# Kernel tuning notes

Hardware: AMD Instinct MI355X
Metric: run time of the kernel (lower is better)

Reference implementation:

```python
import jax, jax.numpy as jnp
import numpy as np

NUM_GRAPHS = 128
NODES_PER_GRAPH = 512
NUM_NODES = NUM_GRAPHS * NODES_PER_GRAPH
NUM_EDGES = NUM_NODES * 16
IN_DIM = 64
HID = 128
NUM_HEADS = 4
BN_EPS = 1e-5


def setup_inputs() -> dict:
    key = jax.random.key(0)
    ks = jax.random.split(key, 12)
    x = jax.random.normal(ks[0], (NUM_NODES, IN_DIM), dtype=jnp.float32)
    edge_index = jax.random.randint(ks[1], (2, NUM_EDGES), 0, NUM_NODES, dtype=jnp.int32)
    batch = jnp.repeat(jnp.arange(NUM_GRAPHS, dtype=jnp.int32), NODES_PER_GRAPH)
    s = 0.05
    W0 = jax.random.normal(ks[2], (IN_DIM, HID), dtype=jnp.float32) * s
    b0 = jnp.zeros((HID,), jnp.float32)
    Wh = jax.random.normal(ks[3], (3, HID, HID), dtype=jnp.float32) * s  # convs 1..3
    bh = jnp.zeros((3, HID), jnp.float32)
    bn_gamma = jnp.ones((4, HID), jnp.float32)
    bn_beta = jnp.zeros((4, HID), jnp.float32)
    bn_mean = jnp.zeros((4, HID), jnp.float32)
    bn_var = jnp.ones((4, HID), jnp.float32)
    attn_in_w = jax.random.normal(ks[4], (3 * HID, HID), dtype=jnp.float32) * s
    attn_in_b = jnp.zeros((3 * HID,), jnp.float32)
    attn_out_w = jax.random.normal(ks[5], (HID, HID), dtype=jnp.float32) * s
    attn_out_b = jnp.zeros((HID,), jnp.float32)
    return dict(x=x, W0=W0, b0=b0, Wh=Wh, bh=bh, bn_gamma=bn_gamma, bn_beta=bn_beta,
                bn_mean=bn_mean, bn_var=bn_var, attn_in_w=attn_in_w, attn_in_b=attn_in_b,
                attn_out_w=attn_out_w, attn_out_b=attn_out_b, edge_index=edge_index, batch=batch)


def _forward(x, W0, b0, Wh, bh, bn_gamma, bn_beta, bn_mean, bn_var,
             attn_in_w, attn_in_b, attn_out_w, attn_out_b, edge_index, batch):
    N = x.shape[0]
    src, dst = edge_index[0], edge_index[1]
    # GCN symmetric normalization with self-loops (PyG GCNConv)
    deg = jax.ops.segment_sum(jnp.ones_like(src, jnp.float32), dst, num_segments=N) + 1.0
    dis = jax.lax.rsqrt(deg)                      # deg^{-1/2}
    enorm = (dis[src] * dis[dst])[:, None]        # per-edge norm
    self_norm = (dis * dis)[:, None]              # self-loop norm

    def gcn(h, W, b):
        h = h @ W
        agg = jax.ops.segment_sum(h[src] * enorm, dst, num_segments=N)
        return agg + h * self_norm + b

    def bn(h, i):
        scale = bn_gamma[i] * jax.lax.rsqrt(bn_var[i] + BN_EPS)
        return (h - bn_mean[i]) * scale + bn_beta[i]  # eval-mode BN

    # dropout is identity in eval mode
    h = jax.nn.relu(bn(gcn(x, W0, b0), 0))
    h = jax.nn.relu(bn(gcn(h, Wh[0], bh[0]), 1))
    h = jax.nn.relu(bn(gcn(h, Wh[1], bh[1]), 2))
    f = jax.nn.relu(bn(gcn(h, Wh[2], bh[2]), 3))   # [N, HID]

    # per-graph self-attention (equal-size contiguous graphs -> batched MHA)
    dh = HID // NUM_HEADS
    xg = f.reshape(NUM_GRAPHS, NODES_PER_GRAPH, HID)
    qkv = xg @ attn_in_w.T + attn_in_b            # [G, n, 3H]
    q, k, v = jnp.split(qkv, 3, axis=-1)

    def heads(t):
        return t.reshape(NUM_GRAPHS, NODES_PER_GRAPH, NUM_HEADS, dh).transpose(0, 2, 1, 3)
    q, k, v = heads(q), heads(k), heads(v)
    scores = jnp.einsum('ghnd,ghmd->ghnm', q, k) / np.sqrt(dh).astype(np.float32)
    attn = jax.nn.softmax(scores, axis=-1)
    o = jnp.einsum('ghnm,ghmd->ghnd', attn, v).transpose(0, 2, 1, 3).reshape(NUM_GRAPHS, NODES_PER_GRAPH, HID)
    o = o @ attn_out_w.T + attn_out_b
    final = o.reshape(N, HID)

    # global mean pool over batch indices
    cnt = jax.ops.segment_sum(jnp.ones((N,), jnp.float32), batch, num_segments=NUM_GRAPHS)
    graph_emb = jax.ops.segment_sum(final, batch, num_segments=NUM_GRAPHS) / cnt[:, None]
    return final, graph_emb


def reference(x, W0, b0, Wh, bh, bn_gamma, bn_beta, bn_mean, bn_var,
              attn_in_w, attn_in_b, attn_out_w, attn_out_b, edge_index, batch):
    return _forward(x, W0, b0, Wh, bh, bn_gamma, bn_beta, bn_mean, bn_var,
                    attn_in_w, attn_in_b, attn_out_w, attn_out_b, edge_index, batch)
```

## Files before the change

kernel.cpp:

```cpp
#include <hip/hip_runtime.h>
#include <hip/hip_bf16.h>
#include <cstdint>
#include <cstddef>

#define N_NODES 65536
#define N_EDGES 1048576
#define N_GRAPHS 128
#define NPG 512
#define IN_DIM 64
#define HID 128
#define BN_EPS 1e-5f

typedef __attribute__((ext_vector_type(8))) short bf16x8;
typedef __attribute__((ext_vector_type(4))) float f32x4;
typedef __attribute__((ext_vector_type(8))) unsigned short u16x8;

__device__ inline unsigned short f2bf(float f) {
  unsigned u = __builtin_bit_cast(unsigned, f);
  u = u + 0x7fffu + ((u >> 16) & 1u);
  return (unsigned short)(u >> 16);
}
__device__ inline float bf2f(unsigned short h) {
  unsigned u = ((unsigned)h) << 16;
  return __builtin_bit_cast(float, u);
}
__device__ inline void split_bf(float v, unsigned short& hi, unsigned short& lo) {
  hi = f2bf(v);
  lo = f2bf(v - bf2f(hi));
}
__device__ inline void split_bf_fast(float v, unsigned short& hi, unsigned short& lo) {
  unsigned u = __builtin_bit_cast(unsigned, v);
  hi = (unsigned short)(u >> 16);
  float r = v - __builtin_bit_cast(float, u & 0xffff0000u);
  lo = f2bf(r);
}

__global__ __launch_bounds__(256) void hist_kernel(const int* __restrict__ dst,
                                                   int* __restrict__ deg) {
  int e = blockIdx.x * 256 + threadIdx.x;
  if (e < N_EDGES) atomicAdd(&deg[dst[e]], 1);
}

__global__ __launch_bounds__(256) void dis_kernel(const int* __restrict__ deg,
                                                  float* __restrict__ dis) {
  int n = blockIdx.x * 256 + threadIdx.x;
  if (n < N_NODES) dis[n] = 1.0f / sqrtf((float)deg[n] + 1.0f);
}

__global__ __launch_bounds__(1024) void scan_kernel(const int* __restrict__ deg,
                                                    int* __restrict__ offsets,
                                                    int* __restrict__ cursor) {
  __shared__ int sums[1024];
  int t = threadIdx.x;
  int base = t * 64;
  const int4* dp = (const int4*)(deg + base);
  int s = 0;
#pragma unroll
  for (int i = 0; i < 16; i++) {
    int4 v = dp[i];
    s += v.x + v.y + v.z + v.w;
  }
  sums[t] = s;
  __syncthreads();
  for (int off = 1; off < 1024; off <<= 1) {
    int v = (t >= off) ? sums[t - off] : 0;
    __syncthreads();
    sums[t] += v;
    __syncthreads();
  }
  int run = (t == 0) ? 0 : sums[t - 1];
#pragma unroll
  for (int i = 0; i < 16; i++) {
    int4 v = dp[i];
    int idx = base + i * 4;
    offsets[idx] = run; cursor[idx] = run; run += v.x;
    offsets[idx + 1] = run; cursor[idx + 1] = run; run += v.y;
    offsets[idx + 2] = run; cursor[idx + 2] = run; run += v.z;
    offsets[idx + 3] = run; cursor[idx + 3] = run; run += v.w;
  }
  if (t == 1023) offsets[N_NODES] = run;
}

__global__ __launch_bounds__(256) void fill_kernel(const int* __restrict__ src,
                                                   const int* __restrict__ dst,
                                                   int* __restrict__ cursor,
                                                   int* __restrict__ csr) {
  int e = blockIdx.x * 256 + threadIdx.x;
  if (e < N_EDGES) {
    int d = dst[e];
    int slot = atomicAdd(&cursor[d], 1);
    csr[slot] = src[e];
  }
}

__global__ __launch_bounds__(256) void agg64_kernel(const float* __restrict__ x,
                                                    const float* __restrict__ dis,
                                                    const int* __restrict__ offsets,
                                                    const int* __restrict__ csr,
                                                    unsigned short* __restrict__ zhi,
                                                    unsigned short* __restrict__ zlo) {
  int node = blockIdx.x * 4 + (threadIdx.x >> 6);
  int lane = threadIdx.x & 63;
  float dn = dis[node];
  float acc = x[(size_t)node * 64 + lane] * dn * dn;
  int beg = offsets[node], end = offsets[node + 1];
  int k = beg;
  for (; k + 4 <= end; k += 4) {
    int s0 = csr[k], s1 = csr[k + 1], s2 = csr[k + 2], s3 = csr[k + 3];
    float w0 = dn * dis[s0], w1 = dn * dis[s1], w2 = dn * dis[s2], w3 = dn * dis[s3];
    float v0 = x[(size_t)s0 * 64 + lane];
    float v1 = x[(size_t)s1 * 64 + lane];
    float v2 = x[(size_t)s2 * 64 + lane];
    float v3 = x[(size_t)s3 * 64 + lane];
    acc = fmaf(w0, v0, acc);
    acc = fmaf(w1, v1, acc);
    acc = fmaf(w2, v2, acc);
    acc = fmaf(w3, v3, acc);
  }
  for (; k < end; k++) {
    int s = csr[k];
    acc = fmaf(dn * dis[s], x[(size_t)s * 64 + lane], acc);
  }
  unsigned short h_, l_;
  split_bf(acc, h_, l_);
  zhi[(size_t)node * 64 + lane] = h_;
  zlo[(size_t)node * 64 + lane] = l_;
}

__global__ __launch_bounds__(256) void agg128_kernel(const float* __restrict__ h,
                                                     const float* __restrict__ dis,
                                                     const int* __restrict__ offsets,
                                                     const int* __restrict__ csr,
                                                     unsigned short* __restrict__ zhi,
                                                     unsigned short* __restrict__ zlo) {
  int node = blockIdx.x * 4 + (threadIdx.x >> 6);
  int lane = threadIdx.x & 63;
  float dn = dis[node];
  float sn = dn * dn;
  const float* hr = h + (size_t)node * 128;
  float a0 = hr[lane] * sn;
  float a1 = hr[lane + 64] * sn;
  int beg = offsets[node], end = offsets[node + 1];
  int k = beg;
  for (; k + 4 <= end; k += 4) {
    int s0 = csr[k], s1 = csr[k + 1], s2 = csr[k + 2], s3 = csr[k + 3];
    float w0 = dn * dis[s0], w1 = dn * dis[s1], w2 = dn * dis[s2], w3 = dn * dis[s3];
    const float* p0 = h + (size_t)s0 * 128;
    const float* p1 = h + (size_t)s1 * 128;
    const float* p2 = h + (size_t)s2 * 128;
    const float* p3 = h + (size_t)s3 * 128;
    float u0 = p0[lane], d0 = p0[lane + 64];
    float u1 = p1[lane], d1 = p1[lane + 64];
    float u2 = p2[lane], d2 = p2[lane + 64];
    float u3 = p3[lane], d3 = p3[lane + 64];
    a0 = fmaf(w0, u0, a0); a1 = fmaf(w0, d0, a1);
    a0 = fmaf(w1, u1, a0); a1 = fmaf(w1, d1, a1);
    a0 = fmaf(w2, u2, a0); a1 = fmaf(w2, d2, a1);
    a0 = fmaf(w3, u3, a0); a1 = fmaf(w3, d3, a1);
  }
  for (; k < end; k++) {
    int s = csr[k];
    float w = dn * dis[s];
    const float* hs = h + (size_t)s * 128;
    a0 = fmaf(w, hs[lane], a0);
    a1 = fmaf(w, hs[lane + 64], a1);
  }
  unsigned short h0, l0, h1, l1;
  split_bf(a0, h0, l0);
  split_bf(a1, h1, l1);
  zhi[(size_t)node * 128 + lane] = h0;
  zlo[(size_t)node * 128 + lane] = l0;
  zhi[(size_t)node * 128 + lane + 64] = h1;
  zlo[(size_t)node * 128 + lane + 64] = l1;
}

template <bool TRANS>
__global__ __launch_bounds__(256) void wprep_kernel(const float* __restrict__ W, int K, int O,
                                                    unsigned short* __restrict__ hi,
                                                    unsigned short* __restrict__ lo) {
  int idx = blockIdx.x * 256 + threadIdx.x;
  int KC = K / 32;
  int total = (O / 16) * KC * 64;
  if (idx >= total) return;
  int lane = idx & 63;
  int rest = idx >> 6;
  int kc = rest % KC;
  int nt = rest / KC;
  int n = nt * 16 + (lane & 15);
  int kb = kc * 32 + (lane >> 4) * 8;
  unsigned short* hp = hi + (size_t)idx * 8;
  unsigned short* lp = lo + (size_t)idx * 8;
#pragma unroll
  for (int j = 0; j < 8; j++) {
    int k = kb + j;
    float v = TRANS ? W[(size_t)n * K + k] : W[(size_t)k * O + n];
    unsigned short h_, l_;
    split_bf(v, h_, l_);
    hp[j] = h_;
    lp[j] = l_;
  }
}

template <int K, int O, bool DOBN, bool DORELU, bool SPLIT_OUT, bool GROUPED>
__global__ __launch_bounds__(256) void gemm_mfma(
    const unsigned short* __restrict__ Ahi, const unsigned short* __restrict__ Alo,
    const unsigned short* __restrict__ Whi, const unsigned short* __restrict__ Wlo,
    const float* __restrict__ bias,
    const float* __restrict__ gamma, const float* __restrict__ beta,
    const float* __restrict__ mean, const float* __restrict__ var,
    float* __restrict__ Cf, unsigned short* __restrict__ Chi,
    unsigned short* __restrict__ Clo) {
  constexpr int KC = K / 32;
  int wave = threadIdx.x >> 6;
  int lane = threadIdx.x & 63;
  int m0 = blockIdx.x * 128 + wave * 32;
  int o0 = blockIdx.y * 128;
  int mrow = lane & 15;
  int kseg = (lane >> 4) * 8;

  f32x4 acc[2][8];
#pragma unroll
  for (int mt = 0; mt < 2; mt++)
#pragma unroll
    for (int nt = 0; nt < 8; nt++) acc[mt][nt] = (f32x4)0.0f;

#pragma unroll
  for (int kc = 0; kc < KC; kc++) {
    bf16x8 ah[2], al[2];
#pragma unroll
    for (int mt = 0; mt < 2; mt++) {
      size_t aoff = (size_t)(m0 + mt * 16 + mrow) * K + kc * 32 + kseg;
      ah[mt] = *(const bf16x8*)(Ahi + aoff);
      al[mt] = *(const bf16x8*)(Alo + aoff);
    }
#pragma unroll
    for (int nt = 0; nt < 8; nt++) {
      size_t foff = (((size_t)(blockIdx.y * 8 + nt) * KC + kc) * 64 + lane) * 8;
      bf16x8 bh = *(const bf16x8*)(Whi + foff);
      bf16x8 bl = *(const bf16x8*)(Wlo + foff);
#pragma unroll
      for (int mt = 0; mt < 2; mt++) {
        acc[mt][nt] = __builtin_amdgcn_mfma_f32_16x16x32_bf16(ah[mt], bh, acc[mt][nt], 0, 0, 0);
        acc[mt][nt] = __builtin_amdgcn_mfma_f32_16x16x32_bf16(ah[mt], bl, acc[mt][nt], 0, 0, 0);
        acc[mt][nt] = __builtin_amdgcn_mfma_f32_16x16x32_bf16(al[mt], bh, acc[mt][nt], 0, 0, 0);
        acc[mt][nt] = __builtin_amdgcn_mfma_f32_16x16x32_bf16(al[mt], bl, acc[mt][nt], 0, 0, 0);
      }
    }
  }

  int ccol = lane & 15;
  int crow0 = (lane >> 4) * 4;
#pragma unroll
  for (int nt = 0; nt < 8; nt++) {
    int c = o0 + nt * 16 + ccol;
    float sc, cb;
    float b = bias[c];
    if (DOBN) {
      sc = gamma[c] * rsqrtf(var[c] + BN_EPS);
      cb = (b - mean[c]) * sc + beta[c];
    } else {
      sc = 1.0f;
      cb = b;
    }
#pragma unroll
    for (int mt = 0; mt < 2; mt++) {
#pragma unroll
      for (int r = 0; r < 4; r++) {
        float v = fmaf(acc[mt][nt][r], sc, cb);
        if (DORELU) v = fmaxf(v, 0.0f);
        size_t row = (size_t)(m0 + mt * 16 + crow0 + r);
        if (SPLIT_OUT) {
          unsigned short h_, l_;
          split_bf(v, h_, l_);
          if (GROUPED) {
            size_t base = row * (size_t)(2 * O) + (size_t)(((c >> 5) << 6) + (c & 31));
            Chi[base] = h_;
            Chi[base + 32] = l_;
          } else {
            Chi[row * O + c] = h_;
            Clo[row * O + c] = l_;
          }
        } else {
          Cf[row * O + c] = v;
        }
      }
    }
  }
}

__global__ __launch_bounds__(256) void knorm_kernel(const unsigned short* __restrict__ qvs,
                                                    float* __restrict__ kmax2) {
  int g = blockIdx.x >> 2;
  int h = blockIdx.x & 3;
  size_t gbase = (size_t)g * NPG;
  float best = 0.0f;
#pragma unroll
  for (int r = 0; r < 2; r++) {
    int j = r * 256 + threadIdx.x;
    size_t base = (gbase + j) * 768 + (size_t)(4 + h) * 64;
    float s = 0.0f;
#pragma unroll
    for (int i = 0; i < 4; i++) {
      u16x8 hh = *(const u16x8*)(qvs + base + i * 8);
      u16x8 ll = *(const u16x8*)(qvs + base + 32 + i * 8);
#pragma unroll
      for (int jj = 0; jj < 8; jj++) {
        float v = bf2f(hh[jj]) + bf2f(ll[jj]);
        s = fmaf(v, v, s);
      }
    }
    best = fmaxf(best, s);
  }
#pragma unroll
  for (int off = 32; off >= 1; off >>= 1)
    best = fmaxf(best, __shfl_xor(best, off, 64));
  __shared__ float red[4];
  int wave = threadIdx.x >> 6;
  if ((threadIdx.x & 63) == 0) red[wave] = best;
  __syncthreads();
  if (threadIdx.x == 0) {
    float m = fmaxf(fmaxf(red[0], red[1]), fmaxf(red[2], red[3]));
    kmax2[blockIdx.x] = m;
  }
}

__global__ __launch_bounds__(256, 2) void attn_mfma_kernel(
    const unsigned short* __restrict__ qvs, const float* __restrict__ kmax2,
    unsigned short* __restrict__ ohi, unsigned short* __restrict__ olo) {
  int wb = ((blockIdx.x & 7) << 7) | (blockIdx.x >> 3);
  int g = wb >> 3;
  int h = (wb >> 1) & 3;
  int half = wb & 1;
  int t = threadIdx.x;
  int wave = t >> 6;
  int lane = t & 63;
  int quad = lane >> 4;
  int l15 = lane & 15;
  size_t gbase = (size_t)g * NPG;
  int qb = half * 256 + wave * 64;

  const float cf = 0.17677669529663687f * 1.4426950408889634f;

  __shared__ unsigned short Kh[2][32][40] __attribute__((aligned(16)));
  __shared__ unsigned short Kl[2][32][40] __attribute__((aligned(16)));
  __shared__ unsigned short Vh[2][33][40] __attribute__((aligned(16)));
  __shared__ unsigned short Vl[2][33][40] __attribute__((aligned(16)));
  __shared__ char wbuf[4][10240] __attribute__((aligned(16)));

  unsigned short* Ph = (unsigned short*)wbuf[wave];
  unsigned short* Pl = Ph + 64 * 40;
  float* Ot = (float*)wbuf[wave];

  bf16x8 qh[4], ql[4];
  float qn2p[4];
#pragma unroll
  for (int mt = 0; mt < 4; mt++) {
    size_t qoff = (gbase + qb + mt * 16 + l15) * 768 + (size_t)h * 64 + quad * 8;
    u16x8 hh = *(const u16x8*)(qvs + qoff);
    u16x8 ll = *(const u16x8*)(qvs + qoff + 32);
    qh[mt] = __builtin_bit_cast(bf16x8, hh);
    ql[mt] = __builtin_bit_cast(bf16x8, ll);
    float s = 0.0f;
#pragma unroll
    for (int j = 0; j < 8; j++) {
      float v = bf2f(hh[j]) + bf2f(ll[j]);
      s = fmaf(v, v, s);
    }
    s += __shfl_xor(s, 16);
    s += __shfl_xor(s, 32);
    qn2p[mt] = s;
  }
  if (quad == 0) {
#pragma unroll
    for (int mt = 0; mt < 4; mt++) Ot[mt * 16 + l15] = qn2p[mt];
  }
  float km2 = kmax2[g * 4 + h];
  float Mq[4][4];
#pragma unroll
  for (int mt = 0; mt < 4; mt++)
#pragma unroll
    for (int r = 0; r < 4; r++)
      Mq[mt][r] = cf * sqrtf(Ot[mt * 16 + quad * 4 + r] * km2);

  f32x4 Oa[4][3];
#pragma unroll
  for (int mt = 0; mt < 4; mt++)
#pragma unroll
    for (int nt = 0; nt < 3; nt++) Oa[mt][nt] = (f32x4)0.0f;

  if (t >= 64 && t < 72) {
    int u = t - 64;
    int bsel = u >> 2;
    int i = u & 3;
    u16x8 ones;
#pragma unroll
    for (int j = 0; j < 8; j++) ones[j] = 0x3F80;
    *(u16x8*)&Vh[bsel][32][i * 8] = ones;
  }

  bool isK = (t >= 128);
  bool isV = (t < 64);
  u16x8 kreg_h, kreg_l;
  ushort4 vreg_h[4], vreg_l[4];
  int kkey = 0, kds = 0, vkeyb = 0, vdvb = 0;
  if (isK) {
    int t2 = t - 128;
    kkey = t2 >> 2;
    kds = (t2 & 3) * 8;
  } else if (isV) {
    vkeyb = (t & 7) * 4;
    vdvb = (t >> 3) * 4;
  }

  auto load_chunk = [&](int c) {
    if (isK) {
      size_t ko = (gbase + (size_t)(c * 32 + kkey)) * 768 + (size_t)(4 + h) * 64 + kds;
      kreg_h = *(const u16x8*)(qvs + ko);
      kreg_l = *(const u16x8*)(qvs + ko + 32);
    } else if (isV) {
#pragma unroll
      for (int r = 0; r < 4; r++) {
        size_t vo = (gbase + (size_t)(c * 32 + vkeyb + r)) * 768 + (size_t)(8 + h) * 64 + vdvb;
        vreg_h[r] = *(const ushort4*)(qvs + vo);
        vreg_l[r] = *(const ushort4*)(qvs + vo + 32);
      }
    }
  };

  auto stage_chunk = [&](int bsel) {
    if (isK) {
      *(u16x8*)&Kh[bsel][kkey][kds] = kreg_h;
      *(u16x8*)&Kl[bsel][kkey][kds] = kreg_l;
    } else if (isV) {
      unsigned short ha[4][4], la[4][4];
#pragma unroll
      for (int r = 0; r < 4; r++) {
        *(ushort4*)&ha[r][0] = vreg_h[r];
        *(ushort4*)&la[r][0] = vreg_l[r];
      }
#pragma unroll
      for (int c2 = 0; c2 < 4; c2++) {
        ushort4 hv, lv;
        hv.x = ha[0][c2]; hv.y = ha[1][c2]; hv.z = ha[2][c2]; hv.w = ha[3][c2];
        lv.x = la[0][c2]; lv.y = la[1][c2]; lv.z = la[2][c2]; lv.w = la[3][c2];
        *(ushort4*)&Vh[bsel][vdvb + c2][vkeyb] = hv;
        *(ushort4*)&Vl[bsel][vdvb + c2][vkeyb] = lv;
      }
    }
  };

  load_chunk(0);
  stage_chunk(0);
  __syncthreads();

  int p = 0;
  for (int c = 0; c < 16; c++) {
    if (c < 15) load_chunk(c + 1);

#pragma unroll
    for (int nt = 0; nt < 2; nt++) {
      bf16x8 bkh = *(const bf16x8*)&Kh[p][nt * 16 + l15][quad * 8];
      bf16x8 bkl = *(const bf16x8*)&Kl[p][nt * 16 + l15][quad * 8];
#pragma unroll
      for (int mt = 0; mt < 4; mt++) {
        f32x4 S = (f32x4)0.0f;
        S = __builtin_amdgcn_mfma_f32_16x16x32_bf16(qh[mt], bkh, S, 0, 0, 0);
        S = __builtin_amdgcn_mfma_f32_16x16x32_bf16(qh[mt], bkl, S, 0, 0, 0);
        S = __builtin_amdgcn_mfma_f32_16x16x32_bf16(ql[mt], bkh, S, 0, 0, 0);
        S = __builtin_amdgcn_mfma_f32_16x16x32_bf16(ql[mt], bkl, S, 0, 0, 0);
#pragma unroll
        for (int r = 0; r < 4; r++) {
          float pexp = __builtin_exp2f(fmaf(S[r], cf, -Mq[mt][r]));
          unsigned short hi_, lo_;
          split_bf_fast(pexp, hi_, lo_);
          int row = mt * 16 + quad * 4 + r;
          Ph[row * 40 + nt * 16 + l15] = hi_;
          Pl[row * 40 + nt * 16 + l15] = lo_;
        }
      }
    }
    bf16x8 pah[4], pal[4];
#pragma unroll
    for (int mt = 0; mt < 4; mt++) {
      pah[mt] = *(const bf16x8*)&Ph[(mt * 16 + l15) * 40 + quad * 8];
      pal[mt] = *(const bf16x8*)&Pl[(mt * 16 + l15) * 40 + quad * 8];
    }
#pragma unroll
    for (int nt = 0; nt < 3; nt++) {
      bf16x8 bvh = *(const bf16x8*)&Vh[p][nt * 16 + l15][quad * 8];
      if (nt < 2) {
        bf16x8 bvl = *(const bf16x8*)&Vl[p][nt * 16 + l15][quad * 8];
#pragma unroll
        for (int mt = 0; mt < 4; mt++) {
          Oa[mt][nt] = __builtin_amdgcn_mfma_f32_16x16x32_bf16(pah[mt], bvh, Oa[mt][nt], 0, 0, 0);
          Oa[mt][nt] = __builtin_amdgcn_mfma_f32_16x16x32_bf16(pah[mt], bvl, Oa[mt][nt], 0, 0, 0);
          Oa[mt][nt] = __builtin_amdgcn_mfma_f32_16x16x32_bf16(pal[mt], bvh, Oa[mt][nt], 0, 0, 0);
        }
      } else {
#pragma unroll
        for (int mt = 0; mt < 4; mt++) {
          Oa[mt][nt] = __builtin_amdgcn_mfma_f32_16x16x32_bf16(pah[mt], bvh, Oa[mt][nt], 0, 0, 0);
          Oa[mt][nt] = __builtin_amdgcn_mfma_f32_16x16x32_bf16(pal[mt], bvh, Oa[mt][nt], 0, 0, 0);
        }
      }
    }

    if (c < 15) stage_chunk(p ^ 1);
    __syncthreads();
    p ^= 1;
  }

#pragma unroll
  for (int mt = 0; mt < 4; mt++) {
#pragma unroll
    for (int r = 0; r < 4; r++) {
      int row = mt * 16 + quad * 4 + r;
      Ot[row * 36 + l15] = Oa[mt][0][r];
      Ot[row * 36 + 16 + l15] = Oa[mt][1][r];
      if (l15 == 0) Ot[row * 36 + 32] = Oa[mt][2][r];
    }
  }
  {
    int row = lane;
    float inv = 1.0f / Ot[row * 36 + 32];
    size_t node = gbase + qb + row;
    u16x8 vh, vl;
#pragma unroll
    for (int seg = 0; seg < 4; seg++) {
#pragma unroll
      for (int j = 0; j < 8; j++) {
        unsigned short hi_, lo_;
        split_bf_fast(Ot[row * 36 + seg * 8 + j] * inv, hi_, lo_);
        vh[j] = hi_;
        vl[j] = lo_;
      }
      *(u16x8*)(ohi + node * 128 + h * 32 + seg * 8) = vh;
      *(u16x8*)(olo + node * 128 + h * 32 + seg * 8) = vl;
    }
  }
}

__global__ __launch_bounds__(128) void pool_kernel(const float* __restrict__ fin,
                                                   float* __restrict__ emb) {
  int g = blockIdx.x >> 2;
  int q = blockIdx.x & 3;
  int c = threadIdx.x;
  const float* p = fin + ((size_t)g * NPG + (size_t)q * 128) * HID + c;
  float s = 0.0f;
#pragma unroll 4
  for (int i = 0; i < 128; i++) s += p[(size_t)i * HID];
  atomicAdd(&emb[g * HID + c], s * (1.0f / NPG));
}

extern "C" void kernel_launch(void* const* d_in, const int* in_sizes, int n_in,
                              void* d_out, int out_size, void* d_ws, size_t ws_size,
                              hipStream_t stream) {
  (void)in_sizes; (void)n_in; (void)out_size; (void)ws_size;
  const float* x          = (const float*)d_in[0];
  const float* W0         = (const float*)d_in[1];
  const float* b0         = (const float*)d_in[2];
  const float* Wh         = (const float*)d_in[3];
  const float* bh         = (const float*)d_in[4];
  const float* bn_gamma   = (const float*)d_in[5];
  const float* bn_beta    = (const float*)d_in[6];
  const float* bn_mean    = (const float*)d_in[7];
  const float* bn_var     = (const float*)d_in[8];
  const float* attn_in_w  = (const float*)d_in[9];
  const float* attn_in_b  = (const float*)d_in[10];
  const float* attn_out_w = (const float*)d_in[11];
  const float* attn_out_b = (const float*)d_in[12];
  const int* edge_index   = (const int*)d_in[13];
  const int* src = edge_index;
  const int* dst = edge_index + N_EDGES;

  char* ws = (char*)d_ws;
  size_t off = 0;
  auto alloc = [&](size_t bytes) -> void* {
    void* p = ws + off;
    off += (bytes + 255) & ~(size_t)255;
    return p;
  };
  int*   deg     = (int*)alloc((size_t)N_NODES * 4);
  int*   offsets = (int*)alloc((size_t)(N_NODES + 1) * 4);
  int*   cursor  = (int*)alloc((size_t)N_NODES * 4);
  int*   csr     = (int*)alloc((size_t)N_EDGES * 4);
  float* dis     = (float*)alloc((size_t)N_NODES * 4);
  float* bufA    = (float*)alloc((size_t)N_NODES * HID * 4);
  unsigned short* zhi = (unsigned short*)alloc((size_t)N_NODES * HID * 2);
  unsigned short* zlo = (unsigned short*)alloc((size_t)N_NODES * HID * 2);
  unsigned short* qvs = (unsigned short*)alloc((size_t)N_NODES * 768 * 2);
  float* kmax2   = (float*)alloc((size_t)N_GRAPHS * 4 * 4);
  unsigned short* w0h = (unsigned short*)alloc(8192 * 2);
  unsigned short* w0l = (unsigned short*)alloc(8192 * 2);
  unsigned short* whh[3], *whl[3];
  for (int i = 0; i < 3; i++) {
    whh[i] = (unsigned short*)alloc(16384 * 2);
    whl[i] = (unsigned short*)alloc(16384 * 2);
  }
  unsigned short* wqh = (unsigned short*)alloc(49152 * 2);
  unsigned short* wql = (unsigned short*)alloc(49152 * 2);
  unsigned short* woh = (unsigned short*)alloc(16384 * 2);
  unsigned short* wol = (unsigned short*)alloc(16384 * 2);

  unsigned short* fhi = (unsigned short*)bufA;
  unsigned short* flo = fhi + (size_t)N_NODES * HID;

  float* fin = (float*)d_out;
  float* emb = fin + (size_t)N_NODES * HID;

  hipMemsetAsync(deg, 0, (size_t)N_NODES * 4, stream);
  hipMemsetAsync(emb, 0, (size_t)N_GRAPHS * HID * 4, stream);
  hist_kernel<<<N_EDGES / 256, 256, 0, stream>>>(dst, deg);
  dis_kernel<<<N_NODES / 256, 256, 0, stream>>>(deg, dis);
  scan_kernel<<<1, 1024, 0, stream>>>(deg, offsets, cursor);
  fill_kernel<<<N_EDGES / 256, 256, 0, stream>>>(src, dst, cursor, csr);

  wprep_kernel<false><<<4, 256, 0, stream>>>(W0, 64, 128, w0h, w0l);
  for (int i = 0; i < 3; i++)
    wprep_kernel<false><<<8, 256, 0, stream>>>(Wh + (size_t)i * HID * HID, 128, 128,
                                               whh[i], whl[i]);
  wprep_kernel<true><<<24, 256, 0, stream>>>(attn_in_w, 128, 384, wqh, wql);
  wprep_kernel<true><<<8, 256, 0, stream>>>(attn_out_w, 128, 128, woh, wol);

  dim3 ggrid(N_NODES / 128, 1);
  agg64_kernel<<<N_NODES / 4, 256, 0, stream>>>(x, dis, offsets, csr, zhi, zlo);
  gemm_mfma<64, 128, true, true, false, false><<<ggrid, 256, 0, stream>>>(
      zhi, zlo, w0h, w0l, b0, bn_gamma, bn_beta, bn_mean, bn_var, bufA, nullptr, nullptr);
  for (int L = 0; L < 2; L++) {
    agg128_kernel<<<N_NODES / 4, 256, 0, stream>>>(bufA, dis, offsets, csr, zhi, zlo);
    gemm_mfma<128, 128, true, true, false, false><<<ggrid, 256, 0, stream>>>(
        zhi, zlo, whh[L], whl[L], bh + (size_t)L * HID,
        bn_gamma + (size_t)(L + 1) * HID, bn_beta + (size_t)(L + 1) * HID,
        bn_mean + (size_t)(L + 1) * HID, bn_var + (size_t)(L + 1) * HID,
        bufA, nullptr, nullptr);
  }
  agg128_kernel<<<N_NODES / 4, 256, 0, stream>>>(bufA, dis, offsets, csr, zhi, zlo);
  gemm_mfma<128, 128, true, true, true, false><<<ggrid, 256, 0, stream>>>(
      zhi, zlo, whh[2], whl[2], bh + (size_t)2 * HID,
      bn_gamma + (size_t)3 * HID, bn_beta + (size_t)3 * HID,
      bn_mean + (size_t)3 * HID, bn_var + (size_t)3 * HID,
      nullptr, fhi, flo);
  dim3 qgrid(N_NODES / 128, 3);
  gemm_mfma<128, 384, false, false, true, true><<<qgrid, 256, 0, stream>>>(
      fhi, flo, wqh, wql, attn_in_b, nullptr, nullptr, nullptr, nullptr,
      nullptr, qvs, nullptr);
  knorm_kernel<<<N_GRAPHS * 4, 256, 0, stream>>>(qvs, kmax2);
  attn_mfma_kernel<<<N_GRAPHS * 4 * 2, 256, 0, stream>>>(qvs, kmax2, zhi, zlo);
  gemm_mfma<128, 128, false, false, false, false><<<ggrid, 256, 0, stream>>>(
      zhi, zlo, woh, wol, attn_out_b, nullptr, nullptr, nullptr, nullptr,
      fin, nullptr, nullptr);
  pool_kernel<<<N_GRAPHS * 4, 128, 0, stream>>>(fin, emb);
}
```

Measured before the change: 823.1 us.

## Fuse mean pooling into output GEMM, pad P tile, add MFMA priority hints

The output projection GEMM now accumulates per-column sums in registers, reduces them across waves through shared memory, and atomically adds the graph means. This removes the separate pool kernel and its re-read of the final activations. In the attention kernel the P staging buffer row stride goes from 40 to 44 halfwords to reduce LDS bank conflicts, and s_setprio raises wave priority around the MFMA sections. The extra shared memory per block may lower occupancy slightly.

```diff
diff --git a/kernel.cpp b/kernel.cpp
--- a/kernel.cpp
+++ b/kernel.cpp
@@ -201,7 +201,8 @@
   }
 }
 
-template <int K, int O, bool DOBN, bool DORELU, bool SPLIT_OUT, bool GROUPED>
+template <int K, int O, bool DOBN, bool DORELU, bool SPLIT_OUT, bool GROUPED,
+          bool DOPOOL = false>
 __global__ __launch_bounds__(256) void gemm_mfma(
     const unsigned short* __restrict__ Ahi, const unsigned short* __restrict__ Alo,
     const unsigned short* __restrict__ Whi, const unsigned short* __restrict__ Wlo,
@@ -209,7 +210,7 @@
     const float* __restrict__ gamma, const float* __restrict__ beta,
     const float* __restrict__ mean, const float* __restrict__ var,
     float* __restrict__ Cf, unsigned short* __restrict__ Chi,
-    unsigned short* __restrict__ Clo) {
+    unsigned short* __restrict__ Clo, float* __restrict__ Pool = nullptr) {
   constexpr int KC = K / 32;
   int wave = threadIdx.x >> 6;
   int lane = threadIdx.x & 63;
@@ -250,6 +251,11 @@
 
   int ccol = lane & 15;
   int crow0 = (lane >> 4) * 4;
+  float colsum[8];
+  if constexpr (DOPOOL) {
+#pragma unroll
+    for (int nt = 0; nt < 8; nt++) colsum[nt] = 0.0f;
+  }
 #pragma unroll
   for (int nt = 0; nt < 8; nt++) {
     int c = o0 + nt * 16 + ccol;
@@ -283,7 +289,25 @@
         } else {
           Cf[row * O + c] = v;
         }
-      }
+        if constexpr (DOPOOL) colsum[nt] += v;
+      }
+    }
+  }
+  if constexpr (DOPOOL) {
+    __shared__ float pb[4][128];
+#pragma unroll
+    for (int nt = 0; nt < 8; nt++) {
+      float cs = colsum[nt];
+      cs += __shfl_xor(cs, 16, 64);
+      cs += __shfl_xor(cs, 32, 64);
+      if ((lane >> 4) == 0) pb[wave][nt * 16 + ccol] = cs;
+    }
+    __syncthreads();
+    int tt = threadIdx.x;
+    if (tt < 128) {
+      float s2 = pb[0][tt] + pb[1][tt] + pb[2][tt] + pb[3][tt];
+      int gg = blockIdx.x >> 2;
+      atomicAdd(&Pool[gg * 128 + tt], s2 * (1.0f / NPG));
     }
   }
 }
@@ -345,10 +369,10 @@
   __shared__ unsigned short Kl[2][32][40] __attribute__((aligned(16)));
   __shared__ unsigned short Vh[2][33][40] __attribute__((aligned(16)));
   __shared__ unsigned short Vl[2][33][40] __attribute__((aligned(16)));
-  __shared__ char wbuf[4][10240] __attribute__((aligned(16)));
+  __shared__ char wbuf[4][11264] __attribute__((aligned(16)));
 
   unsigned short* Ph = (unsigned short*)wbuf[wave];
-  unsigned short* Pl = Ph + 64 * 40;
+  unsigned short* Pl = Ph + 64 * 44;
   float* Ot = (float*)wbuf[wave];
 
   bf16x8 qh[4], ql[4];
@@ -464,27 +488,30 @@
 #pragma unroll
       for (int mt = 0; mt < 4; mt++) {
         f32x4 S = (f32x4)0.0f;
+        __builtin_amdgcn_s_setprio(1);
         S = __builtin_amdgcn_mfma_f32_16x16x32_bf16(qh[mt], bkh, S, 0, 0, 0);
         S = __builtin_amdgcn_mfma_f32_16x16x32_bf16(qh[mt], bkl, S, 0, 0, 0);
         S = __builtin_amdgcn_mfma_f32_16x16x32_bf16(ql[mt], bkh, S, 0, 0, 0);
         S = __builtin_amdgcn_mfma_f32_16x16x32_bf16(ql[mt], bkl, S, 0, 0, 0);
+        __builtin_amdgcn_s_setprio(0);
 #pragma unroll
         for (int r = 0; r < 4; r++) {
           float pexp = __builtin_exp2f(fmaf(S[r], cf, -Mq[mt][r]));
           unsigned short hi_, lo_;
           split_bf_fast(pexp, hi_, lo_);
           int row = mt * 16 + quad * 4 + r;
-          Ph[row * 40 + nt * 16 + l15] = hi_;
-          Pl[row * 40 + nt * 16 + l15] = lo_;
+          Ph[row * 44 + nt * 16 + l15] = hi_;
+          Pl[row * 44 + nt * 16 + l15] = lo_;
         }
       }
     }
     bf16x8 pah[4], pal[4];
 #pragma unroll
     for (int mt = 0; mt < 4; mt++) {
-      pah[mt] = *(const bf16x8*)&Ph[(mt * 16 + l15) * 40 + quad * 8];
-      pal[mt] = *(const bf16x8*)&Pl[(mt * 16 + l15) * 40 + quad * 8];
-    }
+      pah[mt] = *(const bf16x8*)&Ph[(mt * 16 + l15) * 44 + quad * 8];
+      pal[mt] = *(const bf16x8*)&Pl[(mt * 16 + l15) * 44 + quad * 8];
+    }
+    __builtin_amdgcn_s_setprio(1);
 #pragma unroll
     for (int nt = 0; nt < 3; nt++) {
       bf16x8 bvh = *(const bf16x8*)&Vh[p][nt * 16 + l15][quad * 8];
@@ -504,6 +531,7 @@
         }
       }
     }
+    __builtin_amdgcn_s_setprio(0);
 
     if (c < 15) stage_chunk(p ^ 1);
     __syncthreads();
@@ -538,18 +566,6 @@
       *(u16x8*)(olo + node * 128 + h * 32 + seg * 8) = vl;
     }
   }
-}
-
-__global__ __launch_bounds__(128) void pool_kernel(const float* __restrict__ fin,
-                                                   float* __restrict__ emb) {
-  int g = blockIdx.x >> 2;
-  int q = blockIdx.x & 3;
-  int c = threadIdx.x;
-  const float* p = fin + ((size_t)g * NPG + (size_t)q * 128) * HID + c;
-  float s = 0.0f;
-#pragma unroll 4
-  for (int i = 0; i < 128; i++) s += p[(size_t)i * HID];
-  atomicAdd(&emb[g * HID + c], s * (1.0f / NPG));
 }
 
 extern "C" void kernel_launch(void* const* d_in, const int* in_sizes, int n_in,
@@ -646,8 +662,7 @@
       nullptr, qvs, nullptr);
   knorm_kernel<<<N_GRAPHS * 4, 256, 0, stream>>>(qvs, kmax2);
   attn_mfma_kernel<<<N_GRAPHS * 4 * 2, 256, 0, stream>>>(qvs, kmax2, zhi, zlo);
-  gemm_mfma<128, 128, false, false, false, false><<<ggrid, 256, 0, stream>>>(
+  gemm_mfma<128, 128, false, false, false, false, true><<<ggrid, 256, 0, stream>>>(
       zhi, zlo, woh, wol, attn_out_b, nullptr, nullptr, nullptr, nullptr,
-      fin, nullptr, nullptr);
-  pool_kernel<<<N_GRAPHS * 4, 128, 0, stream>>>(fin, emb);
-}
+      fin, nullptr, nullptr, emb);
+}
```

Result: slower. 848.4 us (+3.1%).
